# Kernel tuning notes

Measured on AMD Instinct MI355X. Metric: run time of the kernel, lower is better.

The kernel has to match this reference:

```python
import jax, jax.numpy as jnp
import numpy as np

EPS_DIV = 1e-6    # safe_div clamp
EPS_NORM = 1e-12  # F.normalize eps
EPS_PD = 1e-6     # F.pairwise_distance eps (added to the difference)


def setup_inputs() -> dict:
    key = jax.random.key(0)
    k1, k2, k3 = jax.random.split(key, 3)
    B, N, D, C = 8, 2048, 512, 8192
    x = jax.random.normal(k1, (B, N, D), dtype=jnp.float32)
    W = jax.random.normal(k2, (D, D), dtype=jnp.float32) * (1.0 / np.sqrt(D))
    codebook = jax.random.normal(k3, (C, D), dtype=jnp.float32)
    return {"x": x, "W": W, "codebook": codebook}


def reference(x, W, codebook):
    sg = jax.lax.stop_gradient
    # implicit codebook = Linear(dim, dim, bias=False)(codebook)  -> codebook @ W^T
    imp = codebook @ W.T                                  # [C, D]

    lead = x.shape[:-1]
    D = x.shape[-1]
    xf = x.reshape(-1, D)                                 # [T, D]

    # nearest-neighbor search (no_grad in original): squared-dist argmin == cdist argmin
    d2 = (jnp.sum(xf * xf, axis=-1, keepdims=True)
          - 2.0 * (xf @ imp.T)
          + jnp.sum(imp * imp, axis=-1)[None, :])         # [T, C]
    indices = jnp.argmin(sg(d2), axis=-1)                 # [T]

    qf = imp[indices]                                     # [T, D] gather

    # commit loss: (pairwise_distance(x, q.detach())**2).mean(); torch adds eps to the diff
    diff = xf - sg(qf) + EPS_PD
    commit_loss = jnp.mean(jnp.sum(diff * diff, axis=-1))

    # rotation trick
    norm_x = jnp.linalg.norm(xf, axis=-1, keepdims=True)  # [T, 1]
    norm_q = jnp.linalg.norm(qf, axis=-1, keepdims=True)
    u = xf / jnp.maximum(norm_x, EPS_DIV)
    q = qf / jnp.maximum(norm_q, EPS_DIV)
    s = u + q
    w = sg(s / jnp.maximum(jnp.linalg.norm(s, axis=-1, keepdims=True), EPS_NORM))
    e = xf
    # e - 2 (e.w) w + 2 (e.u_sg) q_sg   (rank-1 products per row)
    rot = (e
           - 2.0 * jnp.sum(e * w, axis=-1, keepdims=True) * w
           + 2.0 * jnp.sum(e * sg(u), axis=-1, keepdims=True) * sg(q))
    quantized = rot * sg(norm_q / jnp.maximum(norm_x, EPS_DIV))

    quantized = quantized.reshape(*lead, D)
    indices = indices.reshape(*lead)
    return quantized, indices, commit_loss
```

## Files before the change

kernel.cpp:

```cpp
#include <hip/hip_runtime.h>
#include <cstdint>
#include <cstddef>

#define DD 512
#define TT 16384
#define CC 8192
#define SPLITC 32
#define EPS_DIV 1e-6f
#define EPS_NORM 1e-12f
#define EPS_PD 1e-6f

typedef _Float16 half8 __attribute__((ext_vector_type(8)));
typedef _Float16 half4 __attribute__((ext_vector_type(4)));
typedef float floatx4 __attribute__((ext_vector_type(4)));

#define GLDS16(g, l) __builtin_amdgcn_global_load_lds( \
    (const __attribute__((address_space(1))) void*)(g), \
    (__attribute__((address_space(3))) void*)(l), 16, 0, 0)

__global__ __launch_bounds__(128) void k_split(const float* __restrict__ src,
                                               _Float16* __restrict__ dst) {
  const int row = blockIdx.x;
  const int col = threadIdx.x * 4;
  float4 v = *(const float4*)(src + (size_t)row * DD + col);
  half4 h, l;
  h.x = (_Float16)v.x; l.x = (_Float16)(v.x - (float)h.x);
  h.y = (_Float16)v.y; l.y = (_Float16)(v.y - (float)h.y);
  h.z = (_Float16)v.z; l.z = (_Float16)(v.z - (float)h.z);
  h.w = (_Float16)v.w; l.w = (_Float16)(v.w - (float)h.w);
  *(half4*)(dst + (size_t)row * 1024 + col) = h;
  *(half4*)(dst + (size_t)row * 1024 + 512 + col) = l;
}

__global__ __launch_bounds__(256) void k_cast_frag(const float* __restrict__ src,
                                                   _Float16* __restrict__ dst) {
  const int rb = blockIdx.x, t = blockIdx.y;
  const int lane = threadIdx.x & 63, s0 = threadIdx.x >> 6;
  const int l15 = lane & 15, quad = lane >> 4;
#pragma unroll
  for (int s = 0; s < 4; ++s) {
    const int slot = s0 * 4 + s;
    const int row = rb * 256 + slot * 16 + l15;
    const float* p = src + (size_t)row * DD + t * 32 + quad * 8;
    float4 v0 = *(const float4*)p;
    float4 v1 = *(const float4*)(p + 4);
    half8 h;
    h[0] = (_Float16)v0.x; h[1] = (_Float16)v0.y;
    h[2] = (_Float16)v0.z; h[3] = (_Float16)v0.w;
    h[4] = (_Float16)v1.x; h[5] = (_Float16)v1.y;
    h[6] = (_Float16)v1.z; h[7] = (_Float16)v1.w;
    *(half8*)(dst + (((size_t)rb * 16 + t) * 16 + slot) * 512 + lane * 8) = h;
  }
}

__global__ __launch_bounds__(256) void k_gemm_mfma(
    const _Float16* __restrict__ cbs, const _Float16* __restrict__ Ws,
    float* __restrict__ imp) {
  __shared__ __align__(16) char smem[65536];
  const int tid = threadIdx.x;
  const int w = tid >> 6, lane = tid & 63;
  const int quad = lane >> 4, l15 = lane & 15;
  const int wm = (w & 1) * 64, wn = (w >> 1) * 64;
  const int c0 = blockIdx.x * 128;
  const int n0 = blockIdx.y * 128;

  const int srow8 = lane >> 3;
  const int scol = ((lane & 7) ^ srow8) << 3;
  size_t arow[4], brow[4];
#pragma unroll
  for (int j = 0; j < 4; ++j) {
    arow[j] = (size_t)(c0 + j * 32 + w * 8 + srow8) * 1024 + scol;
    brow[j] = (size_t)(n0 + j * 32 + w * 8 + srow8) * 1024 + scol;
  }
  int aoff[4], boff[4];
#pragma unroll
  for (int i = 0; i < 4; ++i) {
    aoff[i] = ((wm + i * 16 + l15) * 64 + ((quad ^ (l15 & 7)) << 3)) * 2;
    boff[i] = ((wn + i * 16 + l15) * 64 + ((quad ^ (l15 & 7)) << 3)) * 2;
  }

  auto stage = [&](int buf, int ak, int bk) {
    char* ab = smem + buf * 32768;
    char* bb = ab + 16384;
#pragma unroll
    for (int j = 0; j < 4; ++j) {
      GLDS16(cbs + arow[j] + ak, (_Float16*)ab + (j * 32 + w * 8) * 64);
      GLDS16(Ws  + brow[j] + bk, (_Float16*)bb + (j * 32 + w * 8) * 64);
    }
  };

  floatx4 acc[4][4] = {};
  stage(0, 0, 0);
#pragma unroll 2
  for (int it = 0; it < 24; ++it) {
    __syncthreads();
    if (it < 23) {
      const int n = it + 1;
      const int p = n >> 3, kk = n & 7;
      const int ak = ((p == 2) ? 512 : 0) + kk * 64;
      const int bk = ((p == 1) ? 512 : 0) + kk * 64;
      stage(n & 1, ak, bk);
    }
    const char* ab = smem + (it & 1) * 32768;
    const char* bb = ab + 16384;
#pragma unroll
    for (int ks = 0; ks < 2; ++ks) {
      const int kx = ks * 64;
      half8 a[4], b[4];
#pragma unroll
      for (int mi = 0; mi < 4; ++mi)
        a[mi] = *(const half8*)(ab + (aoff[mi] ^ kx));
#pragma unroll
      for (int ni = 0; ni < 4; ++ni)
        b[ni] = *(const half8*)(bb + (boff[ni] ^ kx));
#pragma unroll
      for (int mi = 0; mi < 4; ++mi)
#pragma unroll
        for (int ni = 0; ni < 4; ++ni)
          acc[mi][ni] = __builtin_amdgcn_mfma_f32_16x16x32_f16(
              a[mi], b[ni], acc[mi][ni], 0, 0, 0);
    }
  }
#pragma unroll
  for (int mi = 0; mi < 4; ++mi)
#pragma unroll
    for (int r = 0; r < 4; ++r) {
      const int c = c0 + wm + mi * 16 + quad * 4 + r;
#pragma unroll
      for (int ni = 0; ni < 4; ++ni) {
        const int d = n0 + wn + ni * 16 + l15;
        imp[(size_t)c * DD + d] = acc[mi][ni][r];
      }
    }
}

__global__ __launch_bounds__(256) void k_row_norm2(
    const float* __restrict__ imp, float* __restrict__ cnorm) {
  const int lane = threadIdx.x & 63;
  const int row = blockIdx.x * 4 + (threadIdx.x >> 6);
  const float* p = imp + (size_t)row * DD + lane * 8;
  float4 a = *(const float4*)p;
  float4 b = *(const float4*)(p + 4);
  float s = a.x * a.x + a.y * a.y + a.z * a.z + a.w * a.w +
            b.x * b.x + b.y * b.y + b.z * b.z + b.w * b.w;
#pragma unroll
  for (int m = 1; m < 64; m <<= 1) s += __shfl_xor(s, m);
  if (lane == 0) cnorm[row] = s;
}

__global__ __launch_bounds__(512, 2) void k_dist_top2(
    const _Float16* __restrict__ xA, const _Float16* __restrict__ ihB,
    const float* __restrict__ cnorm,
    float* __restrict__ bval, int* __restrict__ bidx) {
  __shared__ __align__(16) char smem[131072];
  const int tid = threadIdx.x;
  const int w = tid >> 6, lane = tid & 63;
  const int quad = lane >> 4, l15 = lane & 15;
  const int wr = w >> 2, wc = w & 3;
  const int r0 = blockIdx.x * 256;
  const int c0 = blockIdx.y * 256;

  const _Float16* gA = xA + ((size_t)blockIdx.x * 256 + wr * 8) * 512 + lane * 8;
  const _Float16* gB = ihB + ((size_t)blockIdx.y * 256 + wc * 4) * 512 + lane * 8;

  floatx4 acc[8][4] = {};
  half8 aP[8], bP[4], aQ[8], bQ[4];

#define LOADF(AR, BR, T) {                                                     \
    const _Float16* ga = gA + (size_t)(T) * 8192;                              \
    const _Float16* gb = gB + (size_t)(T) * 8192;                              \
    _Pragma("unroll")                                                          \
    for (int i = 0; i < 8; ++i) AR[i] = *(const half8*)(ga + i * 512);         \
    _Pragma("unroll")                                                          \
    for (int i = 0; i < 4; ++i) BR[i] = *(const half8*)(gb + i * 512);         \
  }
#define MMF(AR, BR) {                                                          \
    __builtin_amdgcn_s_barrier();                                              \
    __builtin_amdgcn_s_setprio(1);                                             \
    _Pragma("unroll")                                                          \
    for (int mi = 0; mi < 8; ++mi)                                             \
      _Pragma("unroll")                                                        \
      for (int ni = 0; ni < 4; ++ni)                                           \
        acc[mi][ni] = __builtin_amdgcn_mfma_f32_16x16x32_f16(                  \
            AR[mi], BR[ni], acc[mi][ni], 0, 0, 0);                             \
    __builtin_amdgcn_s_setprio(0);                                             \
    __builtin_amdgcn_sched_barrier(0);                                         \
  }

  LOADF(aP, bP, 0)
  LOADF(aQ, bQ, 1)   MMF(aP, bP)
  LOADF(aP, bP, 2)   MMF(aQ, bQ)
  LOADF(aQ, bQ, 3)   MMF(aP, bP)
  LOADF(aP, bP, 4)   MMF(aQ, bQ)
  LOADF(aQ, bQ, 5)   MMF(aP, bP)
  LOADF(aP, bP, 6)   MMF(aQ, bQ)
  LOADF(aQ, bQ, 7)   MMF(aP, bP)
  LOADF(aP, bP, 8)   MMF(aQ, bQ)
  LOADF(aQ, bQ, 9)   MMF(aP, bP)
  LOADF(aP, bP, 10)  MMF(aQ, bQ)
  LOADF(aQ, bQ, 11)  MMF(aP, bP)
  LOADF(aP, bP, 12)  MMF(aQ, bQ)
  LOADF(aQ, bQ, 13)  MMF(aP, bP)
  LOADF(aP, bP, 14)  MMF(aQ, bQ)
  LOADF(aQ, bQ, 15)  MMF(aP, bP)
  MMF(aQ, bQ)
#undef LOADF
#undef MMF

  float cn[4];
#pragma unroll
  for (int ni = 0; ni < 4; ++ni)
    cn[ni] = cnorm[c0 + wc * 64 + ni * 16 + l15];

  __syncthreads();
  float* rv = (float*)smem;
  int* ri = (int*)(smem + 65536);
#pragma unroll
  for (int mi = 0; mi < 8; ++mi)
#pragma unroll
    for (int r = 0; r < 4; ++r) {
      const int row = wr * 128 + mi * 16 + quad * 4 + r;
      float bv = 3.4e38f; int bi = 0x7fffffff;
#pragma unroll
      for (int ni = 0; ni < 4; ++ni) {
        const float v = fmaf(-2.0f, acc[mi][ni][r], cn[ni]);
        const int c = c0 + wc * 64 + ni * 16 + l15;
        if (v < bv) { bv = v; bi = c; }
      }
      const int e = wc * 16 + l15;
      const int g = (row & 31) ^ ((row & 4) << 2);
      const int col = e ^ g;
      rv[row * 64 + col] = bv;
      ri[row * 64 + col] = bi;
    }
  __syncthreads();
  {
    const int row = tid >> 1, h = tid & 1;
    const int g = (row & 31) ^ ((row & 4) << 2);
    float v1 = 3.4e38f, v2 = 3.4e38f;
    int i1 = 0x7fffffff, i2 = 0x7fffffff;
#pragma unroll
    for (int j = 0; j < 32; ++j) {
      const int e = h * 32 + j;
      const int col = e ^ g;
      const float v = rv[row * 64 + col];
      const int i = ri[row * 64 + col];
      if (v < v1 || (v == v1 && i < i1)) { v2 = v1; i2 = i1; v1 = v; i1 = i; }
      else if (v < v2 || (v == v2 && i < i2)) { v2 = v; i2 = i; }
    }
    const float w1 = __shfl_xor(v1, 1), w2 = __shfl_xor(v2, 1);
    const int j1 = __shfl_xor(i1, 1), j2 = __shfl_xor(i2, 1);
    if (w1 < v1 || (w1 == v1 && j1 < i1)) {
      if (v1 < w2 || (v1 == w2 && i1 < j2)) { v2 = v1; i2 = i1; }
      else { v2 = w2; i2 = j2; }
      v1 = w1; i1 = j1;
    } else if (w1 < v2 || (w1 == v2 && j1 < i2)) { v2 = w1; i2 = j1; }
    if (h == 0) {
      const size_t o = ((size_t)blockIdx.y * TT + r0 + row) * 2;
      bval[o] = v1; bval[o + 1] = v2;
      bidx[o] = i1; bidx[o + 1] = i2;
    }
  }
}

__global__ __launch_bounds__(256) void k_epilogue(
    const float* __restrict__ x, const float* __restrict__ imp,
    const float* __restrict__ cnorm,
    const float* __restrict__ bval, const int* __restrict__ bidx,
    float* __restrict__ outq, float* __restrict__ outidx,
    float* __restrict__ rloss) {
  const int lane = threadIdx.x & 63;
  const int row = blockIdx.x * 4 + (threadIdx.x >> 6);
  float v1 = 3.4e38f, v2 = 3.4e38f;
  int i1 = 0x7fffffff, i2 = 0x7fffffff;
  if (lane < SPLITC) {
    const size_t o = ((size_t)lane * TT + row) * 2;
    v1 = bval[o]; v2 = bval[o + 1];
    i1 = bidx[o]; i2 = bidx[o + 1];
  }
#pragma unroll
  for (int m = 1; m < 64; m <<= 1) {
    const float w1 = __shfl_xor(v1, m), w2 = __shfl_xor(v2, m);
    const int j1 = __shfl_xor(i1, m), j2 = __shfl_xor(i2, m);
    if (w1 < v1 || (w1 == v1 && j1 < i1)) {
      if (v1 < w2 || (v1 == w2 && i1 < j2)) { v2 = v1; i2 = i1; }
      else { v2 = w2; i2 = j2; }
      v1 = w1; i1 = j1;
    } else {
      if (w1 < v2 || (w1 == v2 && j1 < i2)) { v2 = w1; i2 = j1; }
    }
  }
  const float* xr = x + (size_t)row * DD + lane * 8;
  float e[8], qa[8], qb[8];
  *(float4*)&e[0] = *(const float4*)xr;
  *(float4*)&e[4] = *(const float4*)(xr + 4);
  const float* q1p = imp + (size_t)i1 * DD + lane * 8;
  const float* q2p = imp + (size_t)i2 * DD + lane * 8;
  *(float4*)&qa[0] = *(const float4*)q1p;
  *(float4*)&qa[4] = *(const float4*)(q1p + 4);
  *(float4*)&qb[0] = *(const float4*)q2p;
  *(float4*)&qb[4] = *(const float4*)(q2p + 4);
  float d1 = 0.f, d2 = 0.f;
#pragma unroll
  for (int k = 0; k < 8; ++k) {
    d1 = fmaf(e[k], qa[k], d1);
    d2 = fmaf(e[k], qb[k], d2);
  }
#pragma unroll
  for (int m = 1; m < 64; m <<= 1) {
    d1 += __shfl_xor(d1, m);
    d2 += __shfl_xor(d2, m);
  }
  const float s1 = fmaf(-2.0f, d1, cnorm[i1]);
  const float s2 = fmaf(-2.0f, d2, cnorm[i2]);
  const bool use2 = (s2 < s1) || (s2 == s1 && i2 < i1);
  const int idx = use2 ? i2 : i1;
  float q[8];
#pragma unroll
  for (int k = 0; k < 8; ++k) q[k] = use2 ? qb[k] : qa[k];

  float xx = 0.f, qq = 0.f, xq = 0.f, cl = 0.f;
#pragma unroll
  for (int k = 0; k < 8; ++k) {
    xx = fmaf(e[k], e[k], xx);
    qq = fmaf(q[k], q[k], qq);
    xq = fmaf(e[k], q[k], xq);
    float d = e[k] - q[k] + EPS_PD;
    cl = fmaf(d, d, cl);
  }
#pragma unroll
  for (int m = 1; m < 64; m <<= 1) {
    xx += __shfl_xor(xx, m);
    qq += __shfl_xor(qq, m);
    xq += __shfl_xor(xq, m);
    cl += __shfl_xor(cl, m);
  }
  const float nx = sqrtf(xx), nq = sqrtf(qq);
  const float dx = fmaxf(nx, EPS_DIV), dq = fmaxf(nq, EPS_DIV);
  const float uu = xx / (dx * dx);
  const float qq2 = qq / (dq * dq);
  const float uq = xq / (dx * dq);
  const float ss = uu + qq2 + 2.0f * uq;
  const float dn = fmaxf(sqrtf(ss), EPS_NORM);
  const float es = xx / dx + xq / dq;
  const float a = 2.0f * es / (dn * dn);
  const float b = 2.0f * (xx / dx);
  const float scale = nq / dx;

  float ov[8];
#pragma unroll
  for (int k = 0; k < 8; ++k) {
    const float qp = q[k] / dq;
    const float sk = e[k] / dx + qp;
    ov[k] = (e[k] - a * sk + b * qp) * scale;
  }
  float* op = outq + (size_t)row * DD + lane * 8;
  *(float4*)op = *(const float4*)&ov[0];
  *(float4*)(op + 4) = *(const float4*)&ov[4];
  if (lane == 0) {
    outidx[row] = (float)idx;
    rloss[row] = cl;
  }
}

__global__ __launch_bounds__(256) void k_loss_final(
    const float* __restrict__ rloss, float* __restrict__ out) {
  __shared__ double red[256];
  const int tid = threadIdx.x;
  double s = 0.0;
  for (int i = tid; i < TT; i += 256) s += (double)rloss[i];
  red[tid] = s;
  __syncthreads();
  for (int st = 128; st > 0; st >>= 1) {
    if (tid < st) red[tid] += red[tid + st];
    __syncthreads();
  }
  if (tid == 0) out[0] = (float)(red[0] / (double)TT);
}

extern "C" void kernel_launch(void* const* d_in, const int* in_sizes, int n_in,
                              void* d_out, int out_size, void* d_ws, size_t ws_size,
                              hipStream_t stream) {
  const float* x  = (const float*)d_in[0];
  const float* W  = (const float*)d_in[1];
  const float* cb = (const float*)d_in[2];
  float* out = (float*)d_out;

  float* imp = (float*)d_ws;
  _Float16* ihB = (_Float16*)(imp + (size_t)CC * DD);
  _Float16* cbs = ihB + (size_t)CC * DD;
  _Float16* xA = cbs;
  _Float16* Ws = cbs + (size_t)CC * 1024;
  float* cnorm = (float*)(Ws + (size_t)DD * 1024);
  float* bval  = cnorm + CC;
  int*   bidx  = (int*)(bval + (size_t)SPLITC * TT * 2);
  float* rloss = (float*)(bidx + (size_t)SPLITC * TT * 2);

  float* out_q    = out;
  float* out_idx  = out + (size_t)TT * DD;
  float* out_loss = out_idx + TT;

  k_split<<<CC, 128, 0, stream>>>(cb, cbs);
  k_split<<<DD, 128, 0, stream>>>(W, Ws);
  k_gemm_mfma<<<dim3(CC / 128, DD / 128), 256, 0, stream>>>(cbs, Ws, imp);
  k_row_norm2<<<CC / 4, 256, 0, stream>>>(imp, cnorm);
  k_cast_frag<<<dim3(CC / 256, 16), 256, 0, stream>>>(imp, ihB);
  k_cast_frag<<<dim3(TT / 256, 16), 256, 0, stream>>>(x, xA);
  k_dist_top2<<<dim3(TT / 256, CC / 256), 512, 0, stream>>>(xA, ihB, cnorm, bval, bidx);
  k_epilogue<<<TT / 4, 256, 0, stream>>>(x, imp, cnorm, bval, bidx, out_q, out_idx, rloss);
  k_loss_final<<<1, 256, 0, stream>>>(rloss, out_loss);
}
```

Before: 346.0 us.

## Stage A tiles through LDS with async global_load_lds ring buffer

The distance GEMM's A operand (x rows) is now prefetched three chunks ahead into a 4-slot LDS ring via global_load_lds. Each wave reads its fragments from LDS instead of loading them straight from global into registers. The B operand stays register double-buffered. This reduces register pressure and cuts redundant global loads of A across the four column waves, at the cost of LDS traffic, barriers and hand-tuned vmcnt waits that must match the number of loads in flight.

```diff
diff --git a/kernel.cpp b/kernel.cpp
--- a/kernel.cpp
+++ b/kernel.cpp
@@ -160,52 +160,73 @@
   const int r0 = blockIdx.x * 256;
   const int c0 = blockIdx.y * 256;
 
-  const _Float16* gA = xA + ((size_t)blockIdx.x * 256 + wr * 8) * 512 + lane * 8;
-  const _Float16* gB = ihB + ((size_t)blockIdx.y * 256 + wc * 4) * 512 + lane * 8;
+  const _Float16* gA = xA + (size_t)blockIdx.x * 16 * 8192 + w * 1024 + lane * 8;
+  const _Float16* gB = ihB + (size_t)blockIdx.y * 16 * 8192 + (wc * 4) * 512 + lane * 8;
+  const int ldsDst = w * 2048;
+  const int aBase = (wr * 8) * 1024 + lane * 16;
 
   floatx4 acc[8][4] = {};
-  half8 aP[8], bP[4], aQ[8], bQ[4];
-
-#define LOADF(AR, BR, T) {                                                     \
-    const _Float16* ga = gA + (size_t)(T) * 8192;                              \
-    const _Float16* gb = gB + (size_t)(T) * 8192;                              \
+  half8 aM[8], bP[4], bQ[4];
+
+#define STAGE_A(T) {                                                           \
+    char* d = smem + ((T) & 3) * 16384 + ldsDst;                               \
+    const _Float16* g = gA + (size_t)(T) * 8192;                               \
+    GLDS16(g, d);                                                              \
+    GLDS16(g + 512, d + 1024);                                                 \
+  }
+#define LOAD_B(BR, T) {                                                        \
+    const _Float16* g = gB + (size_t)(T) * 8192;                               \
     _Pragma("unroll")                                                          \
-    for (int i = 0; i < 8; ++i) AR[i] = *(const half8*)(ga + i * 512);         \
+    for (int i = 0; i < 4; ++i) BR[i] = *(const half8*)(g + i * 512);          \
+  }
+
+#define CHUNK(T, BCUR, BNXT, DO_B, DO_G, VMC) {                                \
+    const char* bb = smem + ((T) & 3) * 16384;                                 \
     _Pragma("unroll")                                                          \
-    for (int i = 0; i < 4; ++i) BR[i] = *(const half8*)(gb + i * 512);         \
-  }
-#define MMF(AR, BR) {                                                          \
+    for (int i = 0; i < 8; ++i)                                                \
+      aM[i] = *(const half8*)(bb + aBase + i * 1024);                          \
+    if (DO_B) LOAD_B(BNXT, (T) + 1)                                            \
+    asm volatile("s_waitcnt vmcnt(" #VMC ")" ::: "memory");                    \
     __builtin_amdgcn_s_barrier();                                              \
+    asm volatile("s_waitcnt lgkmcnt(0)" ::: "memory");                         \
+    __builtin_amdgcn_sched_barrier(0);                                         \
+    if (DO_G) STAGE_A((T) + 3)                                                 \
     __builtin_amdgcn_s_setprio(1);                                             \
     _Pragma("unroll")                                                          \
     for (int mi = 0; mi < 8; ++mi)                                             \
       _Pragma("unroll")                                                        \
       for (int ni = 0; ni < 4; ++ni)                                           \
         acc[mi][ni] = __builtin_amdgcn_mfma_f32_16x16x32_f16(                  \
-            AR[mi], BR[ni], acc[mi][ni], 0, 0, 0);                             \
+            aM[mi], BCUR[ni], acc[mi][ni], 0, 0, 0);                           \
     __builtin_amdgcn_s_setprio(0);                                             \
     __builtin_amdgcn_sched_barrier(0);                                         \
   }
 
-  LOADF(aP, bP, 0)
-  LOADF(aQ, bQ, 1)   MMF(aP, bP)
-  LOADF(aP, bP, 2)   MMF(aQ, bQ)
-  LOADF(aQ, bQ, 3)   MMF(aP, bP)
-  LOADF(aP, bP, 4)   MMF(aQ, bQ)
-  LOADF(aQ, bQ, 5)   MMF(aP, bP)
-  LOADF(aP, bP, 6)   MMF(aQ, bQ)
-  LOADF(aQ, bQ, 7)   MMF(aP, bP)
-  LOADF(aP, bP, 8)   MMF(aQ, bQ)
-  LOADF(aQ, bQ, 9)   MMF(aP, bP)
-  LOADF(aP, bP, 10)  MMF(aQ, bQ)
-  LOADF(aQ, bQ, 11)  MMF(aP, bP)
-  LOADF(aP, bP, 12)  MMF(aQ, bQ)
-  LOADF(aQ, bQ, 13)  MMF(aP, bP)
-  LOADF(aP, bP, 14)  MMF(aQ, bQ)
-  LOADF(aQ, bQ, 15)  MMF(aP, bP)
-  MMF(aQ, bQ)
-#undef LOADF
-#undef MMF
+  STAGE_A(0) STAGE_A(1) STAGE_A(2)
+  LOAD_B(bP, 0)
+  asm volatile("s_waitcnt vmcnt(8)" ::: "memory");
+  __builtin_amdgcn_s_barrier();
+  __builtin_amdgcn_sched_barrier(0);
+
+  CHUNK(0,  bP, bQ, 1, 1, 4)
+  CHUNK(1,  bQ, bP, 1, 1, 6)
+  CHUNK(2,  bP, bQ, 1, 1, 6)
+  CHUNK(3,  bQ, bP, 1, 1, 6)
+  CHUNK(4,  bP, bQ, 1, 1, 6)
+  CHUNK(5,  bQ, bP, 1, 1, 6)
+  CHUNK(6,  bP, bQ, 1, 1, 6)
+  CHUNK(7,  bQ, bP, 1, 1, 6)
+  CHUNK(8,  bP, bQ, 1, 1, 6)
+  CHUNK(9,  bQ, bP, 1, 1, 6)
+  CHUNK(10, bP, bQ, 1, 1, 6)
+  CHUNK(11, bQ, bP, 1, 1, 6)
+  CHUNK(12, bP, bQ, 1, 1, 6)
+  CHUNK(13, bQ, bP, 1, 0, 6)
+  CHUNK(14, bP, bQ, 1, 0, 4)
+  CHUNK(15, bQ, bP, 0, 0, 0)
+#undef CHUNK
+#undef STAGE_A
+#undef LOAD_B
 
   float cn[4];
 #pragma unroll
```

Result: faster. 328.5 us (-5.1%).
